# Kernel optimization log

Hardware: AMD Instinct MI355X
Metric: run time of the kernel (lower is better)

Reference implementation:

```python
import jax, jax.numpy as jnp
import numpy as np

N = 100000      # nodes
E = 1600000     # edges (avg degree 16)
IN, HID, OUT = 128, 32, 16
H = 2           # attention heads
EPS = 1e-5
NEG_SLOPE = 0.2


def setup_inputs() -> dict:
    key = jax.random.key(0)
    ks = jax.random.split(key, 24)
    f32 = jnp.float32
    def w(k, shape, scale=0.1):
        return jax.random.normal(k, shape, f32) * scale
    return {
        "x": jax.random.normal(ks[0], (N, IN), f32),
        "edge_index": jax.random.randint(ks[1], (2, E), 0, N, dtype=jnp.int32),
        # GCN layer 1
        "gcn1_W": w(ks[2], (IN, HID)), "gcn1_b": w(ks[3], (HID,)),
        # BN1 (eval mode: running stats)
        "bn1_g": 1.0 + w(ks[4], (HID,)), "bn1_b": w(ks[5], (HID,)),
        "bn1_m": w(ks[6], (HID,)), "bn1_v": 1.0 + jnp.abs(w(ks[7], (HID,))),
        # GAT layer 1 (HID -> HID, heads=H, concat=False)
        "gat1_W": w(ks[8], (HID, H * HID)), "gat1_as": w(ks[9], (H, HID)),
        "gat1_ad": w(ks[10], (H, HID)), "gat1_b": w(ks[11], (HID,)),
        # GCN layer 2
        "gcn2_W": w(ks[12], (HID, HID)), "gcn2_b": w(ks[13], (HID,)),
        # BN2
        "bn2_g": 1.0 + w(ks[14], (HID,)), "bn2_b": w(ks[15], (HID,)),
        "bn2_m": w(ks[16], (HID,)), "bn2_v": 1.0 + jnp.abs(w(ks[17], (HID,))),
        # GAT layer 2 (HID -> OUT, heads=H, concat=False)
        "gat2_W": w(ks[18], (HID, H * OUT)), "gat2_as": w(ks[19], (H, OUT)),
        "gat2_ad": w(ks[20], (H, OUT)), "gat2_b": w(ks[21], (OUT,)),
    }


def _add_self_loops(edge_index):
    loop = jnp.arange(N, dtype=edge_index.dtype)
    src = jnp.concatenate([edge_index[0], loop])
    dst = jnp.concatenate([edge_index[1], loop])
    return src, dst


def _gcn(x, src, dst, W, b):
    h = x @ W                                             # [N, F]
    deg = jax.ops.segment_sum(jnp.ones_like(dst, h.dtype), dst, N)
    dinv = jax.lax.rsqrt(jnp.maximum(deg, 1.0))
    norm = dinv[src] * dinv[dst]                          # [Etot]
    out = jax.ops.segment_sum(h[src] * norm[:, None], dst, N)
    return out + b


def _gat(x, src, dst, W, a_src, a_dst, b, F):
    # PyG GATConv (concat=False -> mean over heads); eval mode (no attn dropout)
    h = (x @ W).reshape(N, H, F)                          # [N, H, F]
    al_s = jnp.einsum('nhf,hf->nh', h, a_src)             # [N, H]
    al_d = jnp.einsum('nhf,hf->nh', h, a_dst)
    e = jax.nn.leaky_relu(al_s[src] + al_d[dst], NEG_SLOPE)  # [Etot, H]
    # segment softmax over destination neighborhoods (self-loops ensure >=1 edge)
    m = jax.ops.segment_max(e, dst, N)
    ex = jnp.exp(e - m[dst])
    s = jax.ops.segment_sum(ex, dst, N)
    alpha = ex / s[dst]                                   # [Etot, H]
    out = jax.ops.segment_sum(alpha[:, :, None] * h[src], dst, N)  # [N, H, F]
    return out.mean(axis=1) + b


def _bn_eval(x, g, b, m, v):
    return (x - m) * jax.lax.rsqrt(v + EPS) * g + b


def reference(x, edge_index, gcn1_W, gcn1_b, bn1_g, bn1_b, bn1_m, bn1_v,
              gat1_W, gat1_as, gat1_ad, gat1_b, gcn2_W, gcn2_b,
              bn2_g, bn2_b, bn2_m, bn2_v, gat2_W, gat2_as, gat2_ad, gat2_b):
    src, dst = _add_self_loops(edge_index)
    h = _gcn(x, src, dst, gcn1_W, gcn1_b)
    h = jax.nn.relu(_bn_eval(h, bn1_g, bn1_b, bn1_m, bn1_v))
    h = jax.nn.relu(_gat(h, src, dst, gat1_W, gat1_as, gat1_ad, gat1_b, HID))
    h = _gcn(h, src, dst, gcn2_W, gcn2_b)
    h = jax.nn.relu(_bn_eval(h, bn2_g, bn2_b, bn2_m, bn2_v))
    h = _gat(h, src, dst, gat2_W, gat2_as, gat2_ad, gat2_b, OUT)
    return jax.nn.log_softmax(h, axis=1)
```

## Files before the change

### kernel.cpp

```cpp
#include <hip/hip_runtime.h>
#include <hip/hip_bf16.h>

#define NN 100000
#define EE 1600000
#define SLAB 64
#define KB 391
#define CHUNK 4096

static constexpr float EPSV = 1e-5f;
static constexpr float SLOPE = 0.2f;

typedef unsigned short ushortt;

__device__ __forceinline__ float lrelu(float v) { return v > 0.f ? v : SLOPE * v; }

__device__ __forceinline__ unsigned rne_bf16(float v) {
    unsigned u = __float_as_uint(v);
    return (u + 0x7fffu + ((u >> 16) & 1u)) >> 16;
}
__device__ __forceinline__ float bf16_lo(unsigned u) { return __uint_as_float(u << 16); }
__device__ __forceinline__ float bf16_hi(unsigned u) { return __uint_as_float(u & 0xffff0000u); }
__device__ __forceinline__ float us2f(ushortt s) { return __uint_as_float((unsigned)s << 16); }


__global__ void k_z(int* __restrict__ hist) {
    int i = threadIdx.x;
    if (i < KB) hist[i] = 0;
}

__global__ __launch_bounds__(256) void k_hist(const int* __restrict__ dst, int* __restrict__ hist) {
    __shared__ int h[KB];
    int tid = threadIdx.x;
    for (int i = tid; i < KB; i += 256) h[i] = 0;
    __syncthreads();
    int e0 = blockIdx.x * CHUNK;
    #pragma unroll
    for (int r = 0; r < CHUNK / 256; ++r) {
        int e = e0 + r * 256 + tid;
        if (e < EE) atomicAdd(&h[dst[e] >> 8], 1);
    }
    __syncthreads();
    for (int i = tid; i < KB; i += 256)
        if (h[i]) atomicAdd(&hist[i], h[i]);
}

__global__ __launch_bounds__(512) void k_scan(const int* __restrict__ hist,
                                              int* __restrict__ start, int* __restrict__ gcur) {
    __shared__ int h[KB];
    int tid = threadIdx.x;
    for (int i = tid; i < KB; i += 512) h[i] = hist[i];
    __syncthreads();
    for (int t = tid; t < KB; t += 512) {
        int s = 0;
        for (int i = 0; i < t; ++i) s += h[i];
        start[t] = s;
        gcur[t] = 0;
    }
}

__global__ __launch_bounds__(256) void k_scat(const int* __restrict__ src, const int* __restrict__ dst,
                                              const int* __restrict__ start, int* __restrict__ gcur,
                                              unsigned int* __restrict__ ebuf) {
    __shared__ int hc[KB], hb[KB];
    int tid = threadIdx.x;
    for (int i = tid; i < KB; i += 256) hc[i] = 0;
    __syncthreads();
    int e0 = blockIdx.x * CHUNK;
    #pragma unroll
    for (int r = 0; r < CHUNK / 256; ++r) {
        int e = e0 + r * 256 + tid;
        if (e < EE) atomicAdd(&hc[dst[e] >> 8], 1);
    }
    __syncthreads();
    for (int i = tid; i < KB; i += 256) {
        int c = hc[i];
        if (c) hb[i] = atomicAdd(&gcur[i], c);
        hc[i] = 0;
    }
    __syncthreads();
    #pragma unroll
    for (int r = 0; r < CHUNK / 256; ++r) {
        int e = e0 + r * 256 + tid;
        if (e < EE) {
            int d = dst[e];
            int b = d >> 8;
            int rk = atomicAdd(&hc[b], 1);
            ebuf[start[b] + hb[b] + rk] = ((unsigned)src[e] << 8) | (unsigned)(d & 255);
        }
    }
}

__global__ __launch_bounds__(256) void k_bucket(const unsigned int* __restrict__ ebuf,
                                                const int* __restrict__ start, const int* __restrict__ hist,
                                                int* __restrict__ col, int* __restrict__ cnt) {
    __shared__ int lc[256];
    int tid = threadIdx.x;
    int b = blockIdx.x;
    lc[tid] = 0;
    __syncthreads();
    int s = start[b], nb = hist[b];
    for (int i = tid; i < nb; i += 256) {
        unsigned v = ebuf[s + i];
        int l = v & 255;
        int r = atomicAdd(&lc[l], 1);
        col[(((b << 8) + l) << 6) + r] = v >> 8;
    }
    __syncthreads();
    int node = (b << 8) + tid;
    if (node < NN) cnt[node] = lc[tid];
}

__global__ void k_deg(const int* __restrict__ cnt, float* __restrict__ dinv,
                      int* __restrict__ col) {
    int i = blockIdx.x * 256 + threadIdx.x;
    if (i < NN) {
        int c = cnt[i];
        dinv[i] = rsqrtf((float)(c + 1));
        col[i * SLAB + c] = i;
    }
}


__global__ __launch_bounds__(256) void k_gemm1(const float* __restrict__ x,
                                               const float* __restrict__ W,
                                               const float* __restrict__ dinv,
                                               ushortt* __restrict__ h) {
    __shared__ float xs[64][128];
    int tid = threadIdx.x;
    int lane = tid & 63;
    int wv = tid >> 6;
    int khalf = lane >> 5, f = lane & 31;
    float wreg[64];
    const float* wp = W + (khalf * 64) * 32 + f;
    #pragma unroll
    for (int i = 0; i < 64; ++i) wreg[i] = wp[i * 32];
    int n0 = blockIdx.x * 64;
    for (int i = tid; i < 64 * 32; i += 256) {
        int row = i >> 5, c4 = i & 31;
        int n = n0 + row;
        float4 v = (n < NN) ? *(const float4*)&x[(size_t)n * 128 + c4 * 4]
                            : make_float4(0.f, 0.f, 0.f, 0.f);
        *(float4*)&xs[row][c4 * 4] = v;
    }
    __syncthreads();
    #pragma unroll 4
    for (int t = 0; t < 16; ++t) {
        int row = wv * 16 + t;
        int n = n0 + row;
        if (n >= NN) break;
        const float* xp = &xs[row][khalf * 64];
        float a0 = 0.f, a1 = 0.f, a2 = 0.f, a3 = 0.f;
        #pragma unroll
        for (int j = 0; j < 16; j += 4) {
            float4 v0 = *(const float4*)&xp[(j + 0) * 4];
            float4 v1 = *(const float4*)&xp[(j + 1) * 4];
            float4 v2 = *(const float4*)&xp[(j + 2) * 4];
            float4 v3 = *(const float4*)&xp[(j + 3) * 4];
            a0 += v0.x * wreg[j * 4 + 0]  + v0.y * wreg[j * 4 + 1]  + v0.z * wreg[j * 4 + 2]  + v0.w * wreg[j * 4 + 3];
            a1 += v1.x * wreg[j * 4 + 4]  + v1.y * wreg[j * 4 + 5]  + v1.z * wreg[j * 4 + 6]  + v1.w * wreg[j * 4 + 7];
            a2 += v2.x * wreg[j * 4 + 8]  + v2.y * wreg[j * 4 + 9]  + v2.z * wreg[j * 4 + 10] + v2.w * wreg[j * 4 + 11];
            a3 += v3.x * wreg[j * 4 + 12] + v3.y * wreg[j * 4 + 13] + v3.z * wreg[j * 4 + 14] + v3.w * wreg[j * 4 + 15];
        }
        float tot = (a0 + a1) + (a2 + a3);
        tot += __shfl_xor(tot, 32);
        if (khalf == 0) h[n * 32 + f] = (ushortt)rne_bf16(tot * dinv[n]);
    }
}


__global__ __launch_bounds__(256) void k_gcn1_gat1t(
    const ushortt* __restrict__ hs, const int* __restrict__ cnt,
    const int* __restrict__ col, const float* __restrict__ dinv,
    const float* __restrict__ gb, const float* __restrict__ bng,
    const float* __restrict__ bnb, const float* __restrict__ bnm,
    const float* __restrict__ bnv,
    const float* __restrict__ W1, const float* __restrict__ as_, const float* __restrict__ ad_,
    unsigned* __restrict__ gp, float* __restrict__ al) {
    __shared__ float wAs[32][32], wBs[32][32];
    int tid = threadIdx.x;
    for (int i = tid; i < 1024; i += 256) {
        int k = i >> 5, f = i & 31;
        wAs[k][f] = W1[k * 64 + f];
        wBs[k][f] = W1[k * 64 + 32 + f];
    }
    __syncthreads();
    int r = tid >> 5, lane = tid & 31;
    int n = blockIdx.x * 8 + r;
    int dn = cnt[n] + 1;
    int base = n * SLAB;
    int c0 = col[base + lane];
    int c1 = col[base + 32 + lane];
    float acc0 = 0.f, acc1 = 0.f, acc2 = 0.f, acc3 = 0.f;
    int j = 0;
    for (; j + 3 < dn; j += 4) {
        int cr0 = (j & 32) ? c1 : c0;
        unsigned a0 = (unsigned)__shfl(cr0, (j + 0) & 31, 32) * 32u + lane;
        unsigned a1 = (unsigned)__shfl(cr0, (j + 1) & 31, 32) * 32u + lane;
        unsigned a2 = (unsigned)__shfl(cr0, (j + 2) & 31, 32) * 32u + lane;
        unsigned a3 = (unsigned)__shfl(cr0, (j + 3) & 31, 32) * 32u + lane;
        acc0 += us2f(hs[a0]);
        acc1 += us2f(hs[a1]);
        acc2 += us2f(hs[a2]);
        acc3 += us2f(hs[a3]);
    }
    for (; j < dn; ++j) {
        unsigned a = (unsigned)__shfl((j & 32) ? c1 : c0, j & 31, 32) * 32u + lane;
        acc0 += us2f(hs[a]);
    }
    float acc = (acc0 + acc1) + (acc2 + acc3);
    float v = dinv[n] * acc + gb[lane];
    v = (v - bnm[lane]) * rsqrtf(bnv[lane] + EPSV) * bng[lane] + bnb[lane];
    v = fmaxf(v, 0.f);
    float gA0 = 0.f, gA1 = 0.f, gB0 = 0.f, gB1 = 0.f;
    #pragma unroll
    for (int k = 0; k < 32; k += 2) {
        float t0 = __shfl(v, k, 32);
        float t1v = __shfl(v, k + 1, 32);
        gA0 += t0 * wAs[k][lane];     gB0 += t0 * wBs[k][lane];
        gA1 += t1v * wAs[k + 1][lane]; gB1 += t1v * wBs[k + 1][lane];
    }
    float gA = gA0 + gA1, gB = gB0 + gB1;
    float pas0 = gA * as_[lane],      pad0 = gA * ad_[lane];
    float pas1 = gB * as_[32 + lane], pad1 = gB * ad_[32 + lane];
    #pragma unroll
    for (int off = 16; off; off >>= 1) {
        pas0 += __shfl_xor(pas0, off);
        pad0 += __shfl_xor(pad0, off);
        pas1 += __shfl_xor(pas1, off);
        pad1 += __shfl_xor(pad1, off);
    }
    if (lane == 0) *(float4*)&al[n * 4] = make_float4(pas0, pas1, pad0, pad1);
    gp[n * 32 + lane] = (rne_bf16(gB) << 16) | rne_bf16(gA);
}


__global__ __launch_bounds__(256) void k_gat1_pv(
    const unsigned* __restrict__ gp, const float* __restrict__ al,
    const int* __restrict__ cnt, const int* __restrict__ col,
    const float* __restrict__ b, const float* __restrict__ W2,
    const float* __restrict__ dinv, ushortt* __restrict__ hs3) {
    __shared__ float2 ec[8][SLAB];
    __shared__ float w2s[32][32];
    int tid = threadIdx.x;
    for (int i = tid; i < 1024; i += 256) w2s[i >> 5][i & 31] = W2[i];
    __syncthreads();
    int r = tid >> 5, lane = tid & 31;
    int n = blockIdx.x * 8 + r;
    int dn = cnt[n] + 1;
    int base = n * SLAB;
    int c0 = col[base + lane];
    int c1 = col[base + 32 + lane];
    float ad0 = al[n * 4 + 2], ad1 = al[n * 4 + 3];
    float e0a = -1e30f, e1a = -1e30f, e0b = -1e30f, e1b = -1e30f;
    if (lane < dn) {
        float4 a4 = *(const float4*)&al[(size_t)c0 * 4];
        e0a = lrelu(a4.x + ad0); e1a = lrelu(a4.y + ad1);
    }
    if (32 + lane < dn) {
        float4 a4 = *(const float4*)&al[(size_t)c1 * 4];
        e0b = lrelu(a4.x + ad0); e1b = lrelu(a4.y + ad1);
    }
    float m0 = fmaxf(e0a, e0b), m1 = fmaxf(e1a, e1b);
    #pragma unroll
    for (int off = 16; off; off >>= 1) {
        m0 = fmaxf(m0, __shfl_xor(m0, off));
        m1 = fmaxf(m1, __shfl_xor(m1, off));
    }
    float x0a = (lane < dn) ? __expf(e0a - m0) : 0.f;
    float x1a = (lane < dn) ? __expf(e1a - m1) : 0.f;
    float x0b = (32 + lane < dn) ? __expf(e0b - m0) : 0.f;
    float x1b = (32 + lane < dn) ? __expf(e1b - m1) : 0.f;
    ec[r][lane] = make_float2(x0a, x1a);
    ec[r][32 + lane] = make_float2(x0b, x1b);
    float s0 = x0a + x0b, s1 = x1a + x1b;
    #pragma unroll
    for (int off = 16; off; off >>= 1) {
        s0 += __shfl_xor(s0, off);
        s1 += __shfl_xor(s1, off);
    }
    float acc00 = 0.f, acc01 = 0.f, acc02 = 0.f, acc03 = 0.f;
    float acc10 = 0.f, acc11 = 0.f, acc12 = 0.f, acc13 = 0.f;
    int j = 0;
    for (; j + 3 < dn; j += 4) {
        int cr = (j & 32) ? c1 : c0;
        unsigned a0 = (unsigned)__shfl(cr, (j + 0) & 31, 32) * 32u + lane;
        unsigned a1 = (unsigned)__shfl(cr, (j + 1) & 31, 32) * 32u + lane;
        unsigned a2 = (unsigned)__shfl(cr, (j + 2) & 31, 32) * 32u + lane;
        unsigned a3 = (unsigned)__shfl(cr, (j + 3) & 31, 32) * 32u + lane;
        unsigned u0 = gp[a0], u1 = gp[a1], u2 = gp[a2], u3 = gp[a3];
        float2 w0 = ec[r][j + 0], w1 = ec[r][j + 1], w2 = ec[r][j + 2], w3 = ec[r][j + 3];
        acc00 += w0.x * bf16_lo(u0); acc10 += w0.y * bf16_hi(u0);
        acc01 += w1.x * bf16_lo(u1); acc11 += w1.y * bf16_hi(u1);
        acc02 += w2.x * bf16_lo(u2); acc12 += w2.y * bf16_hi(u2);
        acc03 += w3.x * bf16_lo(u3); acc13 += w3.y * bf16_hi(u3);
    }
    for (; j < dn; ++j) {
        unsigned a = (unsigned)__shfl((j & 32) ? c1 : c0, j & 31, 32) * 32u + lane;
        unsigned u = gp[a];
        float2 w = ec[r][j];
        acc00 += w.x * bf16_lo(u); acc10 += w.y * bf16_hi(u);
    }
    float a0s = (acc00 + acc01) + (acc02 + acc03);
    float a1s = (acc10 + acc11) + (acc12 + acc13);
    float v = 0.5f * (a0s / s0 + a1s / s1) + b[lane];
    v = fmaxf(v, 0.f);
    float g0 = 0.f, g1 = 0.f;
    #pragma unroll
    for (int k = 0; k < 32; k += 2) {
        g0 += __shfl(v, k, 32) * w2s[k][lane];
        g1 += __shfl(v, k + 1, 32) * w2s[k + 1][lane];
    }
    hs3[n * 32 + lane] = (ushortt)rne_bf16((g0 + g1) * dinv[n]);
}


__global__ __launch_bounds__(256) void k_gcn2_gat2t(
    const ushortt* __restrict__ hs, const int* __restrict__ cnt,
    const int* __restrict__ col, const float* __restrict__ dinv,
    const float* __restrict__ gb, const float* __restrict__ bng,
    const float* __restrict__ bnb, const float* __restrict__ bnm,
    const float* __restrict__ bnv,
    const float* __restrict__ Wg, const float* __restrict__ as_, const float* __restrict__ ad_,
    ushortt* __restrict__ gb16, float* __restrict__ al) {
    __shared__ float wgs[32][32];
    int tid = threadIdx.x;
    for (int i = tid; i < 1024; i += 256) wgs[i >> 5][i & 31] = Wg[i];
    __syncthreads();
    int r = tid >> 5, lane = tid & 31;
    int n = blockIdx.x * 8 + r;
    int dn = cnt[n] + 1;
    int base = n * SLAB;
    int c0 = col[base + lane];
    int c1 = col[base + 32 + lane];
    float acc0 = 0.f, acc1 = 0.f, acc2 = 0.f, acc3 = 0.f;
    int j = 0;
    for (; j + 3 < dn; j += 4) {
        int cr0 = (j & 32) ? c1 : c0;
        unsigned a0 = (unsigned)__shfl(cr0, (j + 0) & 31, 32) * 32u + lane;
        unsigned a1 = (unsigned)__shfl(cr0, (j + 1) & 31, 32) * 32u + lane;
        unsigned a2 = (unsigned)__shfl(cr0, (j + 2) & 31, 32) * 32u + lane;
        unsigned a3 = (unsigned)__shfl(cr0, (j + 3) & 31, 32) * 32u + lane;
        acc0 += us2f(hs[a0]);
        acc1 += us2f(hs[a1]);
        acc2 += us2f(hs[a2]);
        acc3 += us2f(hs[a3]);
    }
    for (; j < dn; ++j) {
        unsigned a = (unsigned)__shfl((j & 32) ? c1 : c0, j & 31, 32) * 32u + lane;
        acc0 += us2f(hs[a]);
    }
    float acc = (acc0 + acc1) + (acc2 + acc3);
    float v = dinv[n] * acc + gb[lane];
    v = (v - bnm[lane]) * rsqrtf(bnv[lane] + EPSV) * bng[lane] + bnb[lane];
    v = fmaxf(v, 0.f);
    float g0 = 0.f, g1 = 0.f;
    #pragma unroll
    for (int k = 0; k < 32; k += 2) {
        g0 += __shfl(v, k, 32) * wgs[k][lane];
        g1 += __shfl(v, k + 1, 32) * wgs[k + 1][lane];
    }
    float g = g0 + g1;
    int hh = lane >> 4, ff = lane & 15;
    float as_v = g * as_[hh * 16 + ff];
    float ad_v = g * ad_[hh * 16 + ff];
    #pragma unroll
    for (int off = 8; off; off >>= 1) {
        as_v += __shfl_xor(as_v, off);
        ad_v += __shfl_xor(ad_v, off);
    }
    if (ff == 0) { al[n * 4 + hh] = as_v; al[n * 4 + 2 + hh] = ad_v; }
    gb16[n * 32 + lane] = (ushortt)rne_bf16(g);
}


__global__ __launch_bounds__(256) void k_gat2_agg(
    const ushortt* __restrict__ gb16, const float* __restrict__ al,
    const int* __restrict__ cnt, const int* __restrict__ col,
    const float* __restrict__ b, float* __restrict__ out) {
    __shared__ float ec[8][2][SLAB];
    int tid = threadIdx.x;
    int r = tid >> 5, lane = tid & 31;
    int n = blockIdx.x * 8 + r;
    int dn = cnt[n] + 1;
    int base = n * SLAB;
    int c0 = col[base + lane];
    int c1 = col[base + 32 + lane];
    float ad0 = al[n * 4 + 2], ad1 = al[n * 4 + 3];
    float e0a = -1e30f, e1a = -1e30f, e0b = -1e30f, e1b = -1e30f;
    if (lane < dn) {
        float4 a4 = *(const float4*)&al[(size_t)c0 * 4];
        e0a = lrelu(a4.x + ad0); e1a = lrelu(a4.y + ad1);
    }
    if (32 + lane < dn) {
        float4 a4 = *(const float4*)&al[(size_t)c1 * 4];
        e0b = lrelu(a4.x + ad0); e1b = lrelu(a4.y + ad1);
    }
    float m0 = fmaxf(e0a, e0b), m1 = fmaxf(e1a, e1b);
    #pragma unroll
    for (int off = 16; off; off >>= 1) {
        m0 = fmaxf(m0, __shfl_xor(m0, off));
        m1 = fmaxf(m1, __shfl_xor(m1, off));
    }
    float x0a = (lane < dn) ? __expf(e0a - m0) : 0.f;
    float x1a = (lane < dn) ? __expf(e1a - m1) : 0.f;
    float x0b = (32 + lane < dn) ? __expf(e0b - m0) : 0.f;
    float x1b = (32 + lane < dn) ? __expf(e1b - m1) : 0.f;
    ec[r][0][lane] = x0a;      ec[r][1][lane] = x1a;
    ec[r][0][32 + lane] = x0b; ec[r][1][32 + lane] = x1b;
    float s0 = x0a + x0b, s1 = x1a + x1b;
    #pragma unroll
    for (int off = 16; off; off >>= 1) {
        s0 += __shfl_xor(s0, off);
        s1 += __shfl_xor(s1, off);
    }
    int hh = lane >> 4, ff = lane & 15;
    const float* ecp = ec[r][hh];
    float acc0 = 0.f, acc1 = 0.f, acc2 = 0.f, acc3 = 0.f;
    int j = 0;
    for (; j + 3 < dn; j += 4) {
        int cr = (j & 32) ? c1 : c0;
        unsigned a0 = (unsigned)__shfl(cr, (j + 0) & 31, 32) * 32u + lane;
        unsigned a1 = (unsigned)__shfl(cr, (j + 1) & 31, 32) * 32u + lane;
        unsigned a2 = (unsigned)__shfl(cr, (j + 2) & 31, 32) * 32u + lane;
        unsigned a3 = (unsigned)__shfl(cr, (j + 3) & 31, 32) * 32u + lane;
        acc0 += ecp[j + 0] * us2f(gb16[a0]);
        acc1 += ecp[j + 1] * us2f(gb16[a1]);
        acc2 += ecp[j + 2] * us2f(gb16[a2]);
        acc3 += ecp[j + 3] * us2f(gb16[a3]);
    }
    for (; j < dn; ++j) {
        unsigned a = (unsigned)__shfl((j & 32) ? c1 : c0, j & 31, 32) * 32u + lane;
        acc0 += ecp[j] * us2f(gb16[a]);
    }
    float acc = ((acc0 + acc1) + (acc2 + acc3)) / (hh ? s1 : s0);
    float v = 0.5f * (acc + __shfl_xor(acc, 16)) + b[ff];
    float mx = v;
    #pragma unroll
    for (int off = 8; off; off >>= 1) mx = fmaxf(mx, __shfl_xor(mx, off));
    float se = __expf(v - mx);
    #pragma unroll
    for (int off = 8; off; off >>= 1) se += __shfl_xor(se, off);
    if (hh == 0) out[(size_t)n * 16 + ff] = v - mx - __logf(se);
}


static inline size_t al256(size_t x) { return (x + 255) & ~((size_t)255); }

extern "C" void kernel_launch(void* const* d_in, const int* in_sizes, int n_in,
                              void* d_out, int out_size, void* d_ws, size_t ws_size,
                              hipStream_t stream) {
    const float* x      = (const float*)d_in[0];
    const int*   ei     = (const int*)d_in[1];
    const float* gcn1_W = (const float*)d_in[2];
    const float* gcn1_b = (const float*)d_in[3];
    const float* bn1_g  = (const float*)d_in[4];
    const float* bn1_b  = (const float*)d_in[5];
    const float* bn1_m  = (const float*)d_in[6];
    const float* bn1_v  = (const float*)d_in[7];
    const float* gat1_W = (const float*)d_in[8];
    const float* gat1_as= (const float*)d_in[9];
    const float* gat1_ad= (const float*)d_in[10];
    const float* gat1_b = (const float*)d_in[11];
    const float* gcn2_W = (const float*)d_in[12];
    const float* gcn2_b = (const float*)d_in[13];
    const float* bn2_g  = (const float*)d_in[14];
    const float* bn2_b  = (const float*)d_in[15];
    const float* bn2_m  = (const float*)d_in[16];
    const float* bn2_v  = (const float*)d_in[17];
    const float* gat2_W = (const float*)d_in[18];
    const float* gat2_as= (const float*)d_in[19];
    const float* gat2_ad= (const float*)d_in[20];
    const float* gat2_b = (const float*)d_in[21];
    float* out = (float*)d_out;

    char* w = (char*)d_ws;
    size_t off = 0;
    auto alloc = [&](size_t bytes) { void* p = w + off; off = al256(off + bytes); return p; };
    int*     cnt   = (int*)alloc((size_t)NN * 4);
    float*   dinv  = (float*)alloc((size_t)NN * 4);
    int*     col   = (int*)alloc((size_t)NN * SLAB * 4);
    ushortt* hsb   = (ushortt*)alloc((size_t)NN * 32 * 2);
    unsigned* g1p  = (unsigned*)alloc((size_t)NN * 32 * 4);
    ushortt* g2b   = (ushortt*)alloc((size_t)NN * 32 * 2);
    float*   al    = (float*)alloc((size_t)NN * 4 * 4);
    int*     hist  = (int*)alloc((size_t)KB * 4);
    int*     start = (int*)alloc((size_t)KB * 4);
    int*     gcur  = (int*)alloc((size_t)KB * 4);
    unsigned int* ebuf = (unsigned int*)g1p;

    const int* esrc = ei;
    const int* edst = ei + EE;
    const int GE = (EE + CHUNK - 1) / CHUNK;

    k_z<<<1, 512, 0, stream>>>(hist);
    k_hist<<<GE, 256, 0, stream>>>(edst, hist);
    k_scan<<<1, 512, 0, stream>>>(hist, start, gcur);
    k_scat<<<GE, 256, 0, stream>>>(esrc, edst, start, gcur, ebuf);
    k_bucket<<<KB, 256, 0, stream>>>(ebuf, start, hist, col, cnt);
    k_deg<<<(NN + 255) / 256, 256, 0, stream>>>(cnt, dinv, col);

    k_gemm1<<<(NN + 63) / 64, 256, 0, stream>>>(x, gcn1_W, dinv, hsb);
    k_gcn1_gat1t<<<NN / 8, 256, 0, stream>>>(hsb, cnt, col, dinv, gcn1_b,
                                             bn1_g, bn1_b, bn1_m, bn1_v,
                                             gat1_W, gat1_as, gat1_ad, g1p, al);
    k_gat1_pv<<<NN / 8, 256, 0, stream>>>(g1p, al, cnt, col, gat1_b,
                                          gcn2_W, dinv, hsb);
    k_gcn2_gat2t<<<NN / 8, 256, 0, stream>>>(hsb, cnt, col, dinv, gcn2_b,
                                             bn2_g, bn2_b, bn2_m, bn2_v,
                                             gat2_W, gat2_as, gat2_ad, g2b, al);
    k_gat2_agg<<<NN / 8, 256, 0, stream>>>(g2b, al, cnt, col, gat2_b, out);
}
```

Before: 302.8 us.

## Pack bf16 feature pairs into 32-bit words and gather two neighbors per wave

Stores intermediate bf16 node features as packed pairs in 32-bit words and switches the four neighbor-aggregation kernels to use half-warps. Each half-warp loads one neighbor's full row with 16 wide loads, so a 32-lane group handles two neighbors per load instead of one, and the second column block is read only when the degree exceeds 32. The aim is fewer, wider gather transactions and fewer loop iterations on the memory-bound edge aggregation. In exchange it adds shuffle-based repacking on writes, cross-half reductions and lane redistribution, plus per-edge predication.

```diff
diff --git a/kernel.cpp b/kernel.cpp
--- a/kernel.cpp
+++ b/kernel.cpp
@@ -10,8 +10,6 @@
 static constexpr float EPSV = 1e-5f;
 static constexpr float SLOPE = 0.2f;
 
-typedef unsigned short ushortt;
-
 __device__ __forceinline__ float lrelu(float v) { return v > 0.f ? v : SLOPE * v; }
 
 __device__ __forceinline__ unsigned rne_bf16(float v) {
@@ -20,7 +18,6 @@
 }
 __device__ __forceinline__ float bf16_lo(unsigned u) { return __uint_as_float(u << 16); }
 __device__ __forceinline__ float bf16_hi(unsigned u) { return __uint_as_float(u & 0xffff0000u); }
-__device__ __forceinline__ float us2f(ushortt s) { return __uint_as_float((unsigned)s << 16); }
 
 
 __global__ void k_z(int* __restrict__ hist) {
@@ -124,7 +121,7 @@
 __global__ __launch_bounds__(256) void k_gemm1(const float* __restrict__ x,
                                                const float* __restrict__ W,
                                                const float* __restrict__ dinv,
-                                               ushortt* __restrict__ h) {
+                                               unsigned* __restrict__ hsp) {
     __shared__ float xs[64][128];
     int tid = threadIdx.x;
     int lane = tid & 63;
@@ -163,13 +160,16 @@
         }
         float tot = (a0 + a1) + (a2 + a3);
         tot += __shfl_xor(tot, 32);
-        if (khalf == 0) h[n * 32 + f] = (ushortt)rne_bf16(tot * dinv[n]);
+        unsigned r16 = rne_bf16(tot * dinv[n]);
+        unsigned hi16 = __shfl(r16, f + 1, 32);
+        if (khalf == 0 && !(f & 1))
+            hsp[n * 16 + (f >> 1)] = (hi16 << 16) | (r16 & 0xffffu);
     }
 }
 
 
 __global__ __launch_bounds__(256) void k_gcn1_gat1t(
-    const ushortt* __restrict__ hs, const int* __restrict__ cnt,
+    const unsigned* __restrict__ hsp, const int* __restrict__ cnt,
     const int* __restrict__ col, const float* __restrict__ dinv,
     const float* __restrict__ gb, const float* __restrict__ bng,
     const float* __restrict__ bnb, const float* __restrict__ bnm,
@@ -185,29 +185,31 @@
     }
     __syncthreads();
     int r = tid >> 5, lane = tid & 31;
+    int half = lane >> 4, l16 = lane & 15;
     int n = blockIdx.x * 8 + r;
     int dn = cnt[n] + 1;
     int base = n * SLAB;
     int c0 = col[base + lane];
-    int c1 = col[base + 32 + lane];
-    float acc0 = 0.f, acc1 = 0.f, acc2 = 0.f, acc3 = 0.f;
-    int j = 0;
-    for (; j + 3 < dn; j += 4) {
-        int cr0 = (j & 32) ? c1 : c0;
-        unsigned a0 = (unsigned)__shfl(cr0, (j + 0) & 31, 32) * 32u + lane;
-        unsigned a1 = (unsigned)__shfl(cr0, (j + 1) & 31, 32) * 32u + lane;
-        unsigned a2 = (unsigned)__shfl(cr0, (j + 2) & 31, 32) * 32u + lane;
-        unsigned a3 = (unsigned)__shfl(cr0, (j + 3) & 31, 32) * 32u + lane;
-        acc0 += us2f(hs[a0]);
-        acc1 += us2f(hs[a1]);
-        acc2 += us2f(hs[a2]);
-        acc3 += us2f(hs[a3]);
-    }
-    for (; j < dn; ++j) {
-        unsigned a = (unsigned)__shfl((j & 32) ? c1 : c0, j & 31, 32) * 32u + lane;
-        acc0 += us2f(hs[a]);
-    }
-    float acc = (acc0 + acc1) + (acc2 + acc3);
+    int c1 = (dn > 32) ? col[base + 32 + lane] : 0;
+    float aL0 = 0.f, aH0 = 0.f, aL1 = 0.f, aH1 = 0.f;
+    for (int j2 = 0; j2 < dn; j2 += 4) {
+        int eA = j2 + half, eB = j2 + 2 + half;
+        int cA = __shfl((j2 < 32) ? c0 : c1, eA & 31, 32);
+        int cB = __shfl((j2 + 2 < 32) ? c0 : c1, eB & 31, 32);
+        bool okA = eA < dn, okB = eB < dn;
+        cA = okA ? cA : 0; cB = okB ? cB : 0;
+        unsigned uA = hsp[cA * 16 + l16];
+        unsigned uB = hsp[cB * 16 + l16];
+        uA = okA ? uA : 0u; uB = okB ? uB : 0u;
+        aL0 += bf16_lo(uA); aH0 += bf16_hi(uA);
+        aL1 += bf16_lo(uB); aH1 += bf16_hi(uB);
+    }
+    float accLo = aL0 + aL1, accHi = aH0 + aH1;
+    accLo += __shfl_xor(accLo, 16);
+    accHi += __shfl_xor(accHi, 16);
+    float vLo = __shfl(accLo, lane >> 1, 32);
+    float vHi = __shfl(accHi, lane >> 1, 32);
+    float acc = (lane & 1) ? vHi : vLo;
     float v = dinv[n] * acc + gb[lane];
     v = (v - bnm[lane]) * rsqrtf(bnv[lane] + EPSV) * bng[lane] + bnb[lane];
     v = fmaxf(v, 0.f);
@@ -238,18 +240,19 @@
     const unsigned* __restrict__ gp, const float* __restrict__ al,
     const int* __restrict__ cnt, const int* __restrict__ col,
     const float* __restrict__ b, const float* __restrict__ W2,
-    const float* __restrict__ dinv, ushortt* __restrict__ hs3) {
+    const float* __restrict__ dinv, unsigned* __restrict__ hs3p) {
     __shared__ float2 ec[8][SLAB];
     __shared__ float w2s[32][32];
     int tid = threadIdx.x;
     for (int i = tid; i < 1024; i += 256) w2s[i >> 5][i & 31] = W2[i];
     __syncthreads();
     int r = tid >> 5, lane = tid & 31;
+    int half = lane >> 4, l16 = lane & 15;
     int n = blockIdx.x * 8 + r;
     int dn = cnt[n] + 1;
     int base = n * SLAB;
     int c0 = col[base + lane];
-    int c1 = col[base + 32 + lane];
+    int c1 = (dn > 32) ? col[base + 32 + lane] : 0;
     float ad0 = al[n * 4 + 2], ad1 = al[n * 4 + 3];
     float e0a = -1e30f, e1a = -1e30f, e0b = -1e30f, e1b = -1e30f;
     if (lane < dn) {
@@ -278,31 +281,35 @@
         s0 += __shfl_xor(s0, off);
         s1 += __shfl_xor(s1, off);
     }
-    float acc00 = 0.f, acc01 = 0.f, acc02 = 0.f, acc03 = 0.f;
-    float acc10 = 0.f, acc11 = 0.f, acc12 = 0.f, acc13 = 0.f;
-    int j = 0;
-    for (; j + 3 < dn; j += 4) {
-        int cr = (j & 32) ? c1 : c0;
-        unsigned a0 = (unsigned)__shfl(cr, (j + 0) & 31, 32) * 32u + lane;
-        unsigned a1 = (unsigned)__shfl(cr, (j + 1) & 31, 32) * 32u + lane;
-        unsigned a2 = (unsigned)__shfl(cr, (j + 2) & 31, 32) * 32u + lane;
-        unsigned a3 = (unsigned)__shfl(cr, (j + 3) & 31, 32) * 32u + lane;
-        unsigned u0 = gp[a0], u1 = gp[a1], u2 = gp[a2], u3 = gp[a3];
-        float2 w0 = ec[r][j + 0], w1 = ec[r][j + 1], w2 = ec[r][j + 2], w3 = ec[r][j + 3];
-        acc00 += w0.x * bf16_lo(u0); acc10 += w0.y * bf16_hi(u0);
-        acc01 += w1.x * bf16_lo(u1); acc11 += w1.y * bf16_hi(u1);
-        acc02 += w2.x * bf16_lo(u2); acc12 += w2.y * bf16_hi(u2);
-        acc03 += w3.x * bf16_lo(u3); acc13 += w3.y * bf16_hi(u3);
-    }
-    for (; j < dn; ++j) {
-        unsigned a = (unsigned)__shfl((j & 32) ? c1 : c0, j & 31, 32) * 32u + lane;
-        unsigned u = gp[a];
-        float2 w = ec[r][j];
-        acc00 += w.x * bf16_lo(u); acc10 += w.y * bf16_hi(u);
-    }
-    float a0s = (acc00 + acc01) + (acc02 + acc03);
-    float a1s = (acc10 + acc11) + (acc12 + acc13);
-    float v = 0.5f * (a0s / s0 + a1s / s1) + b[lane];
+    const uint2* gp2 = (const uint2*)gp;
+    float a0L = 0.f, a0H = 0.f, a1L = 0.f, a1H = 0.f;
+    float b0L = 0.f, b0H = 0.f, b1L = 0.f, b1H = 0.f;
+    for (int j2 = 0; j2 < dn; j2 += 4) {
+        int eA = j2 + half, eB = j2 + 2 + half;
+        int cA = __shfl((j2 < 32) ? c0 : c1, eA & 31, 32);
+        int cB = __shfl((j2 + 2 < 32) ? c0 : c1, eB & 31, 32);
+        bool okA = eA < dn, okB = eB < dn;
+        cA = okA ? cA : 0; cB = okB ? cB : 0;
+        uint2 uA = gp2[cA * 16 + l16];
+        uint2 uB = gp2[cB * 16 + l16];
+        float2 wA = ec[r][eA & 63];
+        float2 wB = ec[r][eB & 63];
+        uA.x = okA ? uA.x : 0u; uA.y = okA ? uA.y : 0u;
+        uB.x = okB ? uB.x : 0u; uB.y = okB ? uB.y : 0u;
+        a0L += wA.x * bf16_lo(uA.x); a1L += wA.y * bf16_hi(uA.x);
+        a0H += wA.x * bf16_lo(uA.y); a1H += wA.y * bf16_hi(uA.y);
+        b0L += wB.x * bf16_lo(uB.x); b1L += wB.y * bf16_hi(uB.x);
+        b0H += wB.x * bf16_lo(uB.y); b1H += wB.y * bf16_hi(uB.y);
+    }
+    a0L += b0L; a0H += b0H; a1L += b1L; a1H += b1H;
+    a0L += __shfl_xor(a0L, 16); a0H += __shfl_xor(a0H, 16);
+    a1L += __shfl_xor(a1L, 16); a1H += __shfl_xor(a1H, 16);
+    int p = lane >> 1;
+    float t0L = __shfl(a0L, p, 32), t0H = __shfl(a0H, p, 32);
+    float t1L = __shfl(a1L, p, 32), t1H = __shfl(a1H, p, 32);
+    float A0 = (lane & 1) ? t0H : t0L;
+    float A1 = (lane & 1) ? t1H : t1L;
+    float v = 0.5f * (A0 / s0 + A1 / s1) + b[lane];
     v = fmaxf(v, 0.f);
     float g0 = 0.f, g1 = 0.f;
     #pragma unroll
@@ -310,46 +317,50 @@
         g0 += __shfl(v, k, 32) * w2s[k][lane];
         g1 += __shfl(v, k + 1, 32) * w2s[k + 1][lane];
     }
-    hs3[n * 32 + lane] = (ushortt)rne_bf16((g0 + g1) * dinv[n]);
+    unsigned r16 = rne_bf16((g0 + g1) * dinv[n]);
+    unsigned hi16 = __shfl(r16, lane + 1, 32);
+    if (!(lane & 1)) hs3p[n * 16 + (lane >> 1)] = (hi16 << 16) | (r16 & 0xffffu);
 }
 
 
 __global__ __launch_bounds__(256) void k_gcn2_gat2t(
-    const ushortt* __restrict__ hs, const int* __restrict__ cnt,
+    const unsigned* __restrict__ hsp, const int* __restrict__ cnt,
     const int* __restrict__ col, const float* __restrict__ dinv,
     const float* __restrict__ gb, const float* __restrict__ bng,
     const float* __restrict__ bnb, const float* __restrict__ bnm,
     const float* __restrict__ bnv,
     const float* __restrict__ Wg, const float* __restrict__ as_, const float* __restrict__ ad_,
-    ushortt* __restrict__ gb16, float* __restrict__ al) {
+    unsigned* __restrict__ g2p, float* __restrict__ al) {
     __shared__ float wgs[32][32];
     int tid = threadIdx.x;
     for (int i = tid; i < 1024; i += 256) wgs[i >> 5][i & 31] = Wg[i];
     __syncthreads();
     int r = tid >> 5, lane = tid & 31;
+    int half = lane >> 4, l16 = lane & 15;
     int n = blockIdx.x * 8 + r;
     int dn = cnt[n] + 1;
     int base = n * SLAB;
     int c0 = col[base + lane];
-    int c1 = col[base + 32 + lane];
-    float acc0 = 0.f, acc1 = 0.f, acc2 = 0.f, acc3 = 0.f;
-    int j = 0;
-    for (; j + 3 < dn; j += 4) {
-        int cr0 = (j & 32) ? c1 : c0;
-        unsigned a0 = (unsigned)__shfl(cr0, (j + 0) & 31, 32) * 32u + lane;
-        unsigned a1 = (unsigned)__shfl(cr0, (j + 1) & 31, 32) * 32u + lane;
-        unsigned a2 = (unsigned)__shfl(cr0, (j + 2) & 31, 32) * 32u + lane;
-        unsigned a3 = (unsigned)__shfl(cr0, (j + 3) & 31, 32) * 32u + lane;
-        acc0 += us2f(hs[a0]);
-        acc1 += us2f(hs[a1]);
-        acc2 += us2f(hs[a2]);
-        acc3 += us2f(hs[a3]);
-    }
-    for (; j < dn; ++j) {
-        unsigned a = (unsigned)__shfl((j & 32) ? c1 : c0, j & 31, 32) * 32u + lane;
-        acc0 += us2f(hs[a]);
-    }
-    float acc = (acc0 + acc1) + (acc2 + acc3);
+    int c1 = (dn > 32) ? col[base + 32 + lane] : 0;
+    float aL0 = 0.f, aH0 = 0.f, aL1 = 0.f, aH1 = 0.f;
+    for (int j2 = 0; j2 < dn; j2 += 4) {
+        int eA = j2 + half, eB = j2 + 2 + half;
+        int cA = __shfl((j2 < 32) ? c0 : c1, eA & 31, 32);
+        int cB = __shfl((j2 + 2 < 32) ? c0 : c1, eB & 31, 32);
+        bool okA = eA < dn, okB = eB < dn;
+        cA = okA ? cA : 0; cB = okB ? cB : 0;
+        unsigned uA = hsp[cA * 16 + l16];
+        unsigned uB = hsp[cB * 16 + l16];
+        uA = okA ? uA : 0u; uB = okB ? uB : 0u;
+        aL0 += bf16_lo(uA); aH0 += bf16_hi(uA);
+        aL1 += bf16_lo(uB); aH1 += bf16_hi(uB);
+    }
+    float accLo = aL0 + aL1, accHi = aH0 + aH1;
+    accLo += __shfl_xor(accLo, 16);
+    accHi += __shfl_xor(accHi, 16);
+    float vLo = __shfl(accLo, lane >> 1, 32);
+    float vHi = __shfl(accHi, lane >> 1, 32);
+    float acc = (lane & 1) ? vHi : vLo;
     float v = dinv[n] * acc + gb[lane];
     v = (v - bnm[lane]) * rsqrtf(bnv[lane] + EPSV) * bng[lane] + bnb[lane];
     v = fmaxf(v, 0.f);
@@ -369,22 +380,25 @@
         ad_v += __shfl_xor(ad_v, off);
     }
     if (ff == 0) { al[n * 4 + hh] = as_v; al[n * 4 + 2 + hh] = ad_v; }
-    gb16[n * 32 + lane] = (ushortt)rne_bf16(g);
+    unsigned r16 = rne_bf16(g);
+    unsigned hi16 = __shfl(r16, lane + 1, 32);
+    if (!(lane & 1)) g2p[n * 16 + (lane >> 1)] = (hi16 << 16) | (r16 & 0xffffu);
 }
 
 
 __global__ __launch_bounds__(256) void k_gat2_agg(
-    const ushortt* __restrict__ gb16, const float* __restrict__ al,
+    const unsigned* __restrict__ g2p, const float* __restrict__ al,
     const int* __restrict__ cnt, const int* __restrict__ col,
     const float* __restrict__ b, float* __restrict__ out) {
-    __shared__ float ec[8][2][SLAB];
+    __shared__ float2 ec[8][SLAB];
     int tid = threadIdx.x;
     int r = tid >> 5, lane = tid & 31;
+    int half = lane >> 4, l16 = lane & 15;
     int n = blockIdx.x * 8 + r;
     int dn = cnt[n] + 1;
     int base = n * SLAB;
     int c0 = col[base + lane];
-    int c1 = col[base + 32 + lane];
+    int c1 = (dn > 32) ? col[base + 32 + lane] : 0;
     float ad0 = al[n * 4 + 2], ad1 = al[n * 4 + 3];
     float e0a = -1e30f, e1a = -1e30f, e0b = -1e30f, e1b = -1e30f;
     if (lane < dn) {
@@ -405,34 +419,40 @@
     float x1a = (lane < dn) ? __expf(e1a - m1) : 0.f;
     float x0b = (32 + lane < dn) ? __expf(e0b - m0) : 0.f;
     float x1b = (32 + lane < dn) ? __expf(e1b - m1) : 0.f;
-    ec[r][0][lane] = x0a;      ec[r][1][lane] = x1a;
-    ec[r][0][32 + lane] = x0b; ec[r][1][32 + lane] = x1b;
+    ec[r][lane] = make_float2(x0a, x1a);
+    ec[r][32 + lane] = make_float2(x0b, x1b);
     float s0 = x0a + x0b, s1 = x1a + x1b;
     #pragma unroll
     for (int off = 16; off; off >>= 1) {
         s0 += __shfl_xor(s0, off);
         s1 += __shfl_xor(s1, off);
     }
+    bool head1 = (l16 & 8) != 0;
+    float aL0 = 0.f, aH0 = 0.f, aL1 = 0.f, aH1 = 0.f;
+    for (int j2 = 0; j2 < dn; j2 += 4) {
+        int eA = j2 + half, eB = j2 + 2 + half;
+        int cA = __shfl((j2 < 32) ? c0 : c1, eA & 31, 32);
+        int cB = __shfl((j2 + 2 < 32) ? c0 : c1, eB & 31, 32);
+        bool okA = eA < dn, okB = eB < dn;
+        cA = okA ? cA : 0; cB = okB ? cB : 0;
+        unsigned uA = g2p[cA * 16 + l16];
+        unsigned uB = g2p[cB * 16 + l16];
+        float2 wA = ec[r][eA & 63];
+        float2 wB = ec[r][eB & 63];
+        float wa = head1 ? wA.y : wA.x;
+        float wb = head1 ? wB.y : wB.x;
+        uA = okA ? uA : 0u; uB = okB ? uB : 0u;
+        aL0 += wa * bf16_lo(uA); aH0 += wa * bf16_hi(uA);
+        aL1 += wb * bf16_lo(uB); aH1 += wb * bf16_hi(uB);
+    }
+    float accLo = aL0 + aL1, accHi = aH0 + aH1;
+    accLo += __shfl_xor(accLo, 16);
+    accHi += __shfl_xor(accHi, 16);
+    float vLo = __shfl(accLo, lane >> 1, 32);
+    float vHi = __shfl(accHi, lane >> 1, 32);
+    float acc = (lane & 1) ? vHi : vLo;
     int hh = lane >> 4, ff = lane & 15;
-    const float* ecp = ec[r][hh];
-    float acc0 = 0.f, acc1 = 0.f, acc2 = 0.f, acc3 = 0.f;
-    int j = 0;
-    for (; j + 3 < dn; j += 4) {
-        int cr = (j & 32) ? c1 : c0;
-        unsigned a0 = (unsigned)__shfl(cr, (j + 0) & 31, 32) * 32u + lane;
-        unsigned a1 = (unsigned)__shfl(cr, (j + 1) & 31, 32) * 32u + lane;
-        unsigned a2 = (unsigned)__shfl(cr, (j + 2) & 31, 32) * 32u + lane;
-        unsigned a3 = (unsigned)__shfl(cr, (j + 3) & 31, 32) * 32u + lane;
-        acc0 += ecp[j + 0] * us2f(gb16[a0]);
-        acc1 += ecp[j + 1] * us2f(gb16[a1]);
-        acc2 += ecp[j + 2] * us2f(gb16[a2]);
-        acc3 += ecp[j + 3] * us2f(gb16[a3]);
-    }
-    for (; j < dn; ++j) {
-        unsigned a = (unsigned)__shfl((j & 32) ? c1 : c0, j & 31, 32) * 32u + lane;
-        acc0 += ecp[j] * us2f(gb16[a]);
-    }
-    float acc = ((acc0 + acc1) + (acc2 + acc3)) / (hh ? s1 : s0);
+    acc /= (hh ? s1 : s0);
     float v = 0.5f * (acc + __shfl_xor(acc, 16)) + b[ff];
     float mx = v;
     #pragma unroll
@@ -476,16 +496,16 @@
     char* w = (char*)d_ws;
     size_t off = 0;
     auto alloc = [&](size_t bytes) { void* p = w + off; off = al256(off + bytes); return p; };
-    int*     cnt   = (int*)alloc((size_t)NN * 4);
-    float*   dinv  = (float*)alloc((size_t)NN * 4);
-    int*     col   = (int*)alloc((size_t)NN * SLAB * 4);
-    ushortt* hsb   = (ushortt*)alloc((size_t)NN * 32 * 2);
-    unsigned* g1p  = (unsigned*)alloc((size_t)NN * 32 * 4);
-    ushortt* g2b   = (ushortt*)alloc((size_t)NN * 32 * 2);
-    float*   al    = (float*)alloc((size_t)NN * 4 * 4);
-    int*     hist  = (int*)alloc((size_t)KB * 4);
-    int*     start = (int*)alloc((size_t)KB * 4);
-    int*     gcur  = (int*)alloc((size_t)KB * 4);
+    int*      cnt   = (int*)alloc((size_t)NN * 4);
+    float*    dinv  = (float*)alloc((size_t)NN * 4);
+    int*      col   = (int*)alloc((size_t)NN * SLAB * 4);
+    unsigned* hsp   = (unsigned*)alloc((size_t)NN * 16 * 4);
+    unsigned* g1p   = (unsigned*)alloc((size_t)NN * 32 * 4);
+    unsigned* g2p   = (unsigned*)alloc((size_t)NN * 16 * 4);
+    float*    al    = (float*)alloc((size_t)NN * 4 * 4);
+    int*      hist  = (int*)alloc((size_t)KB * 4);
+    int*      start = (int*)alloc((size_t)KB * 4);
+    int*      gcur  = (int*)alloc((size_t)KB * 4);
     unsigned int* ebuf = (unsigned int*)g1p;
 
     const int* esrc = ei;
@@ -499,14 +519,14 @@
     k_bucket<<<KB, 256, 0, stream>>>(ebuf, start, hist, col, cnt);
     k_deg<<<(NN + 255) / 256, 256, 0, stream>>>(cnt, dinv, col);
 
-    k_gemm1<<<(NN + 63) / 64, 256, 0, stream>>>(x, gcn1_W, dinv, hsb);
-    k_gcn1_gat1t<<<NN / 8, 256, 0, stream>>>(hsb, cnt, col, dinv, gcn1_b,
+    k_gemm1<<<(NN + 63) / 64, 256, 0, stream>>>(x, gcn1_W, dinv, hsp);
+    k_gcn1_gat1t<<<NN / 8, 256, 0, stream>>>(hsp, cnt, col, dinv, gcn1_b,
                                              bn1_g, bn1_b, bn1_m, bn1_v,
                                              gat1_W, gat1_as, gat1_ad, g1p, al);
     k_gat1_pv<<<NN / 8, 256, 0, stream>>>(g1p, al, cnt, col, gat1_b,
-                                          gcn2_W, dinv, hsb);
-    k_gcn2_gat2t<<<NN / 8, 256, 0, stream>>>(hsb, cnt, col, dinv, gcn2_b,
+                                          gcn2_W, dinv, hsp);
+    k_gcn2_gat2t<<<NN / 8, 256, 0, stream>>>(hsp, cnt, col, dinv, gcn2_b,
                                              bn2_g, bn2_b, bn2_m, bn2_v,
-                                             gat2_W, gat2_as, gat2_ad, g2b, al);
-    k_gat2_agg<<<NN / 8, 256, 0, stream>>>(g2b, al, cnt, col, gat2_b, out);
-}
+                                             gat2_W, gat2_as, gat2_ad, g2p, al);
+    k_gat2_agg<<<NN / 8, 256, 0, stream>>>(g2p, al, cnt, col, gat2_b, out);
+}
```

Measured after the change: 295.8 us. 2.3% less time.
